# Kernel tuning notes

Measured on AMD Instinct MI355X. Metric: run time of the kernel, lower is better.

The kernel has to match this reference:

```python
import jax, jax.numpy as jnp
import numpy as np


def _parallel_scan_affine(log_a, b):
    """Hillis-Steele doubling scan for h_t = a_t*h_{t-1} + b_t (h_0 = 0).

    log_a, b: (B, T, d). Operator: (la2,b2) o (la1,b1) = (la1+la2, exp(la2)*b1 + b2).
    """
    T = log_a.shape[1]
    la, bv = log_a, b
    stride = 1
    while stride < T:  # static Python loop, log2(T) rounds
        la_prev = jnp.roll(la, stride, axis=1).at[:, :stride, :].set(0.0)
        bv_prev = jnp.roll(bv, stride, axis=1).at[:, :stride, :].set(0.0)
        bv = jnp.exp(la) * bv_prev + bv
        la = la + la_prev
        stride *= 2
    return bv


def setup_inputs() -> dict:
    key = jax.random.key(0)
    kx, kwz, kwh = jax.random.split(key, 3)
    B, T, D = 4, 4096, 1024
    x = jax.random.normal(kx, (B, T, D), dtype=jnp.float32)
    # nn.Linear(D, D) weights, stored as (out, in) like torch
    Wz = jax.random.normal(kwz, (D, D), dtype=jnp.float32) * 0.02
    bz = jnp.zeros((D,), dtype=jnp.float32)
    Wh = jax.random.normal(kwh, (D, D), dtype=jnp.float32) * 0.02
    bh = jnp.zeros((D,), dtype=jnp.float32)
    return {"x": x, "Wz": Wz, "bz": bz, "Wh": Wh, "bh": bh}


def reference(x, Wz, bz, Wh, bh):
    # forward_parallel: z = sigmoid(linear_z(x)); h_tilde = linear_h(x)
    z = jax.nn.sigmoid(jnp.einsum("btd,ed->bte", x, Wz) + bz)
    h_tilde = jnp.einsum("btd,ed->bte", x, Wh) + bh
    log_a = jnp.log(1.0 - z + 1e-08)
    b = z * h_tilde
    h_out = _parallel_scan_affine(log_a, b)
    return h_out  # out_proj is Identity since d_inner == d_model
```

## Files before the change

### kernel.cpp

```cpp
#include <hip/hip_runtime.h>
#include <hip/hip_bf16.h>


typedef __bf16 bf16x8 __attribute__((ext_vector_type(8)));
typedef __bf16 bf16x4 __attribute__((ext_vector_type(4)));
typedef float  f32x4  __attribute__((ext_vector_type(4)));

#define BSZ 4
#define TSZ 4096
#define DSZ 1024
#define MSZ (BSZ*TSZ)
#define CH  16
#define NC  (TSZ/CH)

__device__ __forceinline__ void gload_lds16(const __bf16* g, __bf16* l) {
  __builtin_amdgcn_global_load_lds(
      (const __attribute__((address_space(1))) void*)g,
      (__attribute__((address_space(3))) void*)l, 16, 0, 0);
}

__global__ void convert_tile_kernel(const float* __restrict__ X,
                                    const float* __restrict__ Wz,
                                    const float* __restrict__ Wh,
                                    __bf16* __restrict__ Xc,
                                    __bf16* __restrict__ Wzc,
                                    __bf16* __restrict__ Whc)
{
  const int bx = blockIdx.x;
  const float* src; __bf16* dst; int gid;
  if (bx < 8192)      { src = X;  dst = Xc;  gid =  bx        *256 + threadIdx.x; }
  else if (bx < 8704) { src = Wz; dst = Wzc; gid = (bx - 8192)*256 + threadIdx.x; }
  else                { src = Wh; dst = Whc; gid = (bx - 8704)*256 + threadIdx.x; }
  const int l    = gid & 63;
  const int i    = (gid >> 6) & 7;
  const int kblk = (gid >> 9) & 31;
  const int rblk = gid >> 14;
  const int row  = rblk*128 + i*16 + (l & 15);
  const int col  = kblk*32 + (l >> 4)*8;
  const float* g = src + (size_t)row*DSZ + col;
  float4 v0 = *(const float4*)g;
  float4 v1 = *(const float4*)(g + 4);
  bf16x8 p;
  p[0]=(__bf16)v0.x; p[1]=(__bf16)v0.y; p[2]=(__bf16)v0.z; p[3]=(__bf16)v0.w;
  p[4]=(__bf16)v1.x; p[5]=(__bf16)v1.y; p[6]=(__bf16)v1.z; p[7]=(__bf16)v1.w;
  *(bf16x8*)(dst + (size_t)gid*8) = p;
}

__global__ __launch_bounds__(256, 2) void gemm_gate_kernel(
    const __bf16* __restrict__ Xc,  const __bf16* __restrict__ Wzc,
    const __bf16* __restrict__ Whc,
    const float* __restrict__ bz, const float* __restrict__ bh,
    __bf16* __restrict__ a_ws, float* __restrict__ b_out,
    float* __restrict__ Aprod, float* __restrict__ Bcomp)
{
  __shared__ __align__(16) __bf16 As [8192];
  __shared__ __align__(16) __bf16 Bzs[8192];
  __shared__ __align__(16) __bf16 Bhs[8192];

  const int tid  = threadIdx.x;
  const int lane = tid & 63;
  const int wv   = tid >> 6;
  const int wM   = (wv >> 1) * 64;
  const int wN   = (wv & 1) * 64;
  const int wMg  = wM >> 4;
  const int wNg  = wN >> 4;
  const int lr   = lane & 15;
  const int q    = lane >> 4;
  const int wbase = wv * 64;

  const __bf16* Xb = Xc  + (size_t)blockIdx.x * 32 * 4096;
  const __bf16* Zb = Wzc + (size_t)blockIdx.y * 32 * 4096;
  const __bf16* Hb = Whc + (size_t)blockIdx.y * 32 * 4096;

  f32x4 accz[4][4] = {};
  f32x4 acch[4][4] = {};

  for (int kblk = 0; kblk < 16; ++kblk) {
    __syncthreads();
    const size_t tb = (size_t)kblk * 8192;
    #pragma unroll
    for (int c = 0; c < 4; ++c) {
      const int eo = (c*256 + wbase + lane) * 8;
      const int lo = (c*256 + wbase) * 8;
      gload_lds16(Xb + tb + eo, As  + lo);
      gload_lds16(Zb + tb + eo, Bzs + lo);
      gload_lds16(Hb + tb + eo, Bhs + lo);
    }
    __syncthreads();

    #pragma unroll
    for (int h = 0; h < 2; ++h) {
      const int ho = h * 4096;
      bf16x8 af[4];
      #pragma unroll
      for (int i = 0; i < 4; ++i)
        af[i] = *(const bf16x8*)(As + ho + (wMg + i)*512 + lane*8);
      #pragma unroll
      for (int j = 0; j < 4; ++j) {
        bf16x8 bz8 = *(const bf16x8*)(Bzs + ho + (wNg + j)*512 + lane*8);
        bf16x8 bh8 = *(const bf16x8*)(Bhs + ho + (wNg + j)*512 + lane*8);
        #pragma unroll
        for (int i = 0; i < 4; ++i) {
          accz[j][i] = __builtin_amdgcn_mfma_f32_16x16x32_bf16(af[i], bz8, accz[j][i], 0, 0, 0);
          acch[j][i] = __builtin_amdgcn_mfma_f32_16x16x32_bf16(af[i], bh8, acch[j][i], 0, 0, 0);
        }
      }
    }
  }

  const int M0 = blockIdx.x * 128;
  const int N0 = blockIdx.y * 128;
  #pragma unroll
  for (int j = 0; j < 4; ++j) {
    const int e = N0 + wN + j*16 + lr;
    const float bzv = bz[e];
    const float bhv = bh[e];
    float Aseg[4], Bseg[4];
    #pragma unroll
    for (int i = 0; i < 4; ++i) {
      const int mbase = M0 + wM + i*16 + q*4;
      float A = 1.0f, Bv = 0.0f;
      #pragma unroll
      for (int r = 0; r < 4; ++r) {
        const size_t idx = (size_t)(mbase + r)*DSZ + e;
        const float pz = accz[j][i][r] + bzv;
        const float ph = acch[j][i][r] + bhv;
        const float ex = __expf(-pz);
        const float z  = 1.0f / (1.0f + ex);
        const __bf16 abf = (__bf16)fmaf(ex, z, 1e-8f);
        const float  af  = (float)abf;
        const float  bf  = z * ph;
        a_ws[idx]  = abf;
        b_out[idx] = bf;
        Bv = fmaf(af, Bv, bf);
        A *= af;
      }
      Aseg[i] = A; Bseg[i] = Bv;
    }
    #pragma unroll
    for (int i = 0; i < 4; ++i) {
      #pragma unroll
      for (int s = 16; s < 64; s <<= 1) {
        const float Ap = __shfl_up(Aseg[i], s, 64);
        const float Bp = __shfl_up(Bseg[i], s, 64);
        if (lane >= s) { Bseg[i] = fmaf(Aseg[i], Bp, Bseg[i]); Aseg[i] *= Ap; }
      }
    }
    if (q == 3) {
      #pragma unroll
      for (int i = 0; i < 4; ++i) {
        const int bc = (M0 + wM + i*16) >> 4;
        Aprod[(size_t)bc*DSZ + e] = Aseg[i];
        Bcomp[(size_t)bc*DSZ + e] = Bseg[i];
      }
    }
  }
}

#define P2B 16
__global__ void scan_pass2_kernel(const float* Aprod,
                                  const float* __restrict__ Bcomp,
                                  float* Hstart)
{
  const int lane = threadIdx.x & 63;
  const int b    = blockIdx.x >> 4;
  const int d    = (blockIdx.x & 15) * 64 + lane;
  const size_t base = (size_t)b * NC * DSZ + d;
  float h = 0.0f;
  for (int c0 = 0; c0 < NC; c0 += P2B) {
    float Ar[P2B], Br[P2B];
    #pragma unroll
    for (int c = 0; c < P2B; ++c) {
      Ar[c] = Aprod[base + (size_t)(c0 + c)*DSZ];
      Br[c] = Bcomp[base + (size_t)(c0 + c)*DSZ];
    }
    #pragma unroll
    for (int c = 0; c < P2B; ++c) {
      Hstart[base + (size_t)(c0 + c)*DSZ] = h;
      h = fmaf(Ar[c], h, Br[c]);
    }
  }
}

__global__ void scan_pass3_kernel(const __bf16* __restrict__ a_ws,
                                  const float* __restrict__ Hstart,
                                  float* __restrict__ out)
{
  const int bc   = blockIdx.x;
  const int d0   = threadIdx.x * 4;
  const size_t base = (size_t)bc * CH * DSZ + d0;
  float4 hv = *(const float4*)(Hstart + (size_t)bc*DSZ + d0);
  float h[4] = {hv.x, hv.y, hv.z, hv.w};
  #pragma unroll
  for (int t = 0; t < CH; ++t) {
    bf16x4 a4 = *(const bf16x4*)(a_ws + base + (size_t)t*DSZ);
    float4 b4 = *(const float4*)(out + base + (size_t)t*DSZ);
    const float bb[4] = {b4.x, b4.y, b4.z, b4.w};
    #pragma unroll
    for (int c = 0; c < 4; ++c)
      h[c] = fmaf((float)a4[c], h[c], bb[c]);
    *(float4*)(out + base + (size_t)t*DSZ) = make_float4(h[0], h[1], h[2], h[3]);
  }
}

extern "C" void kernel_launch(void* const* d_in, const int* in_sizes, int n_in,
                              void* d_out, int out_size, void* d_ws, size_t ws_size,
                              hipStream_t stream)
{
  const float* x  = (const float*)d_in[0];
  const float* Wz = (const float*)d_in[1];
  const float* bz = (const float*)d_in[2];
  const float* Wh = (const float*)d_in[3];
  const float* bh = (const float*)d_in[4];
  float* out = (float*)d_out;

  __bf16* Xc   = (__bf16*)d_ws;
  __bf16* Wzc  = Xc  + (size_t)MSZ * DSZ;
  __bf16* Whc  = Wzc + (size_t)DSZ * DSZ;
  __bf16* a_ws = Whc + (size_t)DSZ * DSZ;
  float* Aprod  = (float*)(a_ws + (size_t)MSZ * DSZ);
  float* Bcomp  = Aprod + (size_t)BSZ*NC*DSZ;
  float* Hstart = Aprod;

  convert_tile_kernel<<<9216, 256, 0, stream>>>(x, Wz, Wh, Xc, Wzc, Whc);
  gemm_gate_kernel<<<dim3(MSZ/128, DSZ/128), 256, 0, stream>>>(
      Xc, Wzc, Whc, bz, bh, a_ws, out, Aprod, Bcomp);
  scan_pass2_kernel<<<64, 64, 0, stream>>>(Aprod, Bcomp, Hstart);
  scan_pass3_kernel<<<BSZ*NC, 256, 0, stream>>>(a_ws, Hstart, out);
}
```

Before: 241.3 us.

## Restructure gate GEMM into 256x256 double-buffered tiles with interleaved Wz/Wh

Wz and Wh are interleaved into one combined weight matrix in 16-row groups, so the GEMM treats the two projections as a single N=2048 product. The GEMM kernel moves to 512-thread blocks computing 256x256 tiles, with double-buffered LDS loads prefetched a step ahead and explicit vmcnt waits and barriers. It also raises MFMA priority with s_setprio and remaps block indices for L2 locality. This is meant to hide global-to-LDS latency and improve operand reuse, at the cost of more LDS (128KB per block), higher register pressure and hand-managed synchronisation that must be exactly right.

```diff
diff --git a/kernel.cpp b/kernel.cpp
--- a/kernel.cpp
+++ b/kernel.cpp
@@ -10,8 +10,12 @@
 #define TSZ 4096
 #define DSZ 1024
 #define MSZ (BSZ*TSZ)
+#define NSZ 2048
 #define CH  16
 #define NC  (TSZ/CH)
+
+#define BAR()  asm volatile("s_barrier" ::: "memory")
+#define VMW(n) asm volatile("s_waitcnt vmcnt(" #n ")" ::: "memory")
 
 __device__ __forceinline__ void gload_lds16(const __bf16* g, __bf16* l) {
   __builtin_amdgcn_global_load_lds(
@@ -23,19 +27,24 @@
                                     const float* __restrict__ Wz,
                                     const float* __restrict__ Wh,
                                     __bf16* __restrict__ Xc,
-                                    __bf16* __restrict__ Wzc,
-                                    __bf16* __restrict__ Whc)
+                                    __bf16* __restrict__ Wc)
 {
   const int bx = blockIdx.x;
-  const float* src; __bf16* dst; int gid;
-  if (bx < 8192)      { src = X;  dst = Xc;  gid =  bx        *256 + threadIdx.x; }
-  else if (bx < 8704) { src = Wz; dst = Wzc; gid = (bx - 8192)*256 + threadIdx.x; }
-  else                { src = Wh; dst = Whc; gid = (bx - 8704)*256 + threadIdx.x; }
+  const float* src; __bf16* dst; int gid; int row;
+  if (bx < 8192) {
+    gid = bx*256 + threadIdx.x;
+    const int l = gid & 63, i = (gid >> 6) & 7, rblk = gid >> 14;
+    row = rblk*128 + i*16 + (l & 15);
+    src = X; dst = Xc;
+  } else {
+    gid = (bx - 8192)*256 + threadIdx.x;
+    const int l = gid & 63, i = (gid >> 6) & 7, rblk = gid >> 14;
+    const int g = rblk*8 + i;
+    row = (g >> 1)*16 + (l & 15);
+    src = (g & 1) ? Wh : Wz; dst = Wc;
+  }
   const int l    = gid & 63;
-  const int i    = (gid >> 6) & 7;
   const int kblk = (gid >> 9) & 31;
-  const int rblk = gid >> 14;
-  const int row  = rblk*128 + i*16 + (l & 15);
   const int col  = kblk*32 + (l >> 4)*8;
   const float* g = src + (size_t)row*DSZ + col;
   float4 v0 = *(const float4*)g;
@@ -46,85 +55,147 @@
   *(bf16x8*)(dst + (size_t)gid*8) = p;
 }
 
-__global__ __launch_bounds__(256, 2) void gemm_gate_kernel(
-    const __bf16* __restrict__ Xc,  const __bf16* __restrict__ Wzc,
-    const __bf16* __restrict__ Whc,
+__global__ __launch_bounds__(512, 2) void gemm_gate_kernel(
+    const __bf16* __restrict__ Xc, const __bf16* __restrict__ Wc,
     const float* __restrict__ bz, const float* __restrict__ bh,
     __bf16* __restrict__ a_ws, float* __restrict__ b_out,
     float* __restrict__ Aprod, float* __restrict__ Bcomp)
 {
-  __shared__ __align__(16) __bf16 As [8192];
-  __shared__ __align__(16) __bf16 Bzs[8192];
-  __shared__ __align__(16) __bf16 Bhs[8192];
+  __shared__ __align__(16) __bf16 As[32768];
+  __shared__ __align__(16) __bf16 Bs[32768];
 
   const int tid  = threadIdx.x;
   const int lane = tid & 63;
-  const int wv   = tid >> 6;
-  const int wM   = (wv >> 1) * 64;
-  const int wN   = (wv & 1) * 64;
-  const int wMg  = wM >> 4;
-  const int wNg  = wN >> 4;
+  const int w    = tid >> 6;
+  const int wr   = w >> 2;
+  const int wc   = w & 3;
   const int lr   = lane & 15;
   const int q    = lane >> 4;
-  const int wbase = wv * 64;
-
-  const __bf16* Xb = Xc  + (size_t)blockIdx.x * 32 * 4096;
-  const __bf16* Zb = Wzc + (size_t)blockIdx.y * 32 * 4096;
-  const __bf16* Hb = Whc + (size_t)blockIdx.y * 32 * 4096;
-
-  f32x4 accz[4][4] = {};
-  f32x4 acch[4][4] = {};
-
-  for (int kblk = 0; kblk < 16; ++kblk) {
-    __syncthreads();
-    const size_t tb = (size_t)kblk * 8192;
-    #pragma unroll
-    for (int c = 0; c < 4; ++c) {
-      const int eo = (c*256 + wbase + lane) * 8;
-      const int lo = (c*256 + wbase) * 8;
-      gload_lds16(Xb + tb + eo, As  + lo);
-      gload_lds16(Zb + tb + eo, Bzs + lo);
-      gload_lds16(Hb + tb + eo, Bhs + lo);
-    }
-    __syncthreads();
-
-    #pragma unroll
-    for (int h = 0; h < 2; ++h) {
-      const int ho = h * 4096;
-      bf16x8 af[4];
-      #pragma unroll
-      for (int i = 0; i < 4; ++i)
-        af[i] = *(const bf16x8*)(As + ho + (wMg + i)*512 + lane*8);
-      #pragma unroll
-      for (int j = 0; j < 4; ++j) {
-        bf16x8 bz8 = *(const bf16x8*)(Bzs + ho + (wNg + j)*512 + lane*8);
-        bf16x8 bh8 = *(const bf16x8*)(Bhs + ho + (wNg + j)*512 + lane*8);
-        #pragma unroll
-        for (int i = 0; i < 4; ++i) {
-          accz[j][i] = __builtin_amdgcn_mfma_f32_16x16x32_bf16(af[i], bz8, accz[j][i], 0, 0, 0);
-          acch[j][i] = __builtin_amdgcn_mfma_f32_16x16x32_bf16(af[i], bh8, acch[j][i], 0, 0, 0);
-        }
-      }
-    }
-  }
-
-  const int M0 = blockIdx.x * 128;
-  const int N0 = blockIdx.y * 128;
-  #pragma unroll
-  for (int j = 0; j < 4; ++j) {
-    const int e = N0 + wN + j*16 + lr;
+
+  const int bid = blockIdx.x;
+  const int wg  = (bid & 7)*64 + (bid >> 3);
+  const int bx  = wg >> 3;
+  const int by  = wg & 7;
+
+  const int    lgo   = tid * 8;
+  const int    llo   = (tid >> 6) * 512;
+  const size_t xbase = (size_t)bx * 262144 + lgo;
+  const size_t wbase = (size_t)by * 262144 + lgo;
+  const int ard   = wr*4096 + lane*8;
+  const int bbase = (wc >> 1)*4096 + (wc & 1)*2048 + lane*8;
+
+  f32x4 acc[8][4] = {};
+  bf16x8 a4[4], b4[4];
+
+  #pragma unroll
+  for (int h = 0; h < 2; ++h) gload_lds16(Xc + xbase + h*131072 + 0*4096, As + 0*8192 + h*4096 + llo);
+  #pragma unroll
+  for (int h = 0; h < 2; ++h) gload_lds16(Wc + wbase + h*131072 + 0*4096, Bs + 0*8192 + h*4096 + llo);
+  #pragma unroll
+  for (int h = 0; h < 2; ++h) gload_lds16(Xc + xbase + h*131072 + 1*4096, As + 1*8192 + h*4096 + llo);
+  #pragma unroll
+  for (int h = 0; h < 2; ++h) gload_lds16(Wc + wbase + h*131072 + 1*4096, Bs + 1*8192 + h*4096 + llo);
+  VMW(4);
+  BAR();
+
+  for (int t = 0; t < 16; ++t) {
+    const int cur = t & 1, nxt = cur ^ 1;
+    const int cb0 = (cur*2 + 0)*8192;
+    const int cb1 = (cur*2 + 1)*8192;
+    const int nb0 = (nxt*2 + 0)*8192;
+    const int nb1 = (nxt*2 + 1)*8192;
+    const size_t g0 = (size_t)(2*t + 2) * 4096;
+    const size_t g1 = (size_t)(2*t + 3) * 4096;
+
+    #pragma unroll
+    for (int m = 0; m < 4; ++m) a4[m] = *(const bf16x8*)(As + cb0 + ard + m*512);
+    #pragma unroll
+    for (int j = 0; j < 4; ++j) b4[j] = *(const bf16x8*)(Bs + cb0 + bbase + j*512);
+    if (t < 15) {
+      #pragma unroll
+      for (int h = 0; h < 2; ++h) gload_lds16(Xc + xbase + h*131072 + g0, As + nb0 + h*4096 + llo);
+    }
+    BAR();
+    __builtin_amdgcn_s_setprio(1);
+    #pragma unroll
+    for (int j = 0; j < 4; ++j)
+      #pragma unroll
+      for (int m = 0; m < 4; ++m)
+        acc[m][j] = __builtin_amdgcn_mfma_f32_16x16x32_bf16(a4[m], b4[j], acc[m][j], 0, 0, 0);
+    __builtin_amdgcn_s_setprio(0);
+    BAR();
+
+    #pragma unroll
+    for (int m = 0; m < 4; ++m) a4[m] = *(const bf16x8*)(As + cb0 + ard + (4+m)*512);
+    if (t < 15) {
+      #pragma unroll
+      for (int h = 0; h < 2; ++h) gload_lds16(Wc + wbase + h*131072 + g0, Bs + nb0 + h*4096 + llo);
+      VMW(4);
+    } else {
+      VMW(0);
+    }
+    BAR();
+    __builtin_amdgcn_s_setprio(1);
+    #pragma unroll
+    for (int j = 0; j < 4; ++j)
+      #pragma unroll
+      for (int m = 0; m < 4; ++m)
+        acc[4+m][j] = __builtin_amdgcn_mfma_f32_16x16x32_bf16(a4[m], b4[j], acc[4+m][j], 0, 0, 0);
+    __builtin_amdgcn_s_setprio(0);
+    BAR();
+
+    #pragma unroll
+    for (int m = 0; m < 4; ++m) a4[m] = *(const bf16x8*)(As + cb1 + ard + m*512);
+    #pragma unroll
+    for (int j = 0; j < 4; ++j) b4[j] = *(const bf16x8*)(Bs + cb1 + bbase + j*512);
+    if (t < 15) {
+      #pragma unroll
+      for (int h = 0; h < 2; ++h) gload_lds16(Xc + xbase + h*131072 + g1, As + nb1 + h*4096 + llo);
+    }
+    BAR();
+    __builtin_amdgcn_s_setprio(1);
+    #pragma unroll
+    for (int j = 0; j < 4; ++j)
+      #pragma unroll
+      for (int m = 0; m < 4; ++m)
+        acc[m][j] = __builtin_amdgcn_mfma_f32_16x16x32_bf16(a4[m], b4[j], acc[m][j], 0, 0, 0);
+    __builtin_amdgcn_s_setprio(0);
+    BAR();
+
+    #pragma unroll
+    for (int m = 0; m < 4; ++m) a4[m] = *(const bf16x8*)(As + cb1 + ard + (4+m)*512);
+    if (t < 15) {
+      #pragma unroll
+      for (int h = 0; h < 2; ++h) gload_lds16(Wc + wbase + h*131072 + g1, Bs + nb1 + h*4096 + llo);
+      VMW(4);
+    }
+    BAR();
+    __builtin_amdgcn_s_setprio(1);
+    #pragma unroll
+    for (int j = 0; j < 4; ++j)
+      #pragma unroll
+      for (int m = 0; m < 4; ++m)
+        acc[4+m][j] = __builtin_amdgcn_mfma_f32_16x16x32_bf16(a4[m], b4[j], acc[4+m][j], 0, 0, 0);
+    __builtin_amdgcn_s_setprio(0);
+    BAR();
+  }
+
+  const int rowb = bx*256 + wr*128;
+  #pragma unroll
+  for (int u = 0; u < 2; ++u) {
+    const int e = (by*8 + wc*2 + u)*16 + lr;
     const float bzv = bz[e];
     const float bhv = bh[e];
-    float Aseg[4], Bseg[4];
-    #pragma unroll
-    for (int i = 0; i < 4; ++i) {
-      const int mbase = M0 + wM + i*16 + q*4;
+    float Aseg[8], Bseg[8];
+    #pragma unroll
+    for (int m = 0; m < 8; ++m) {
+      const int mbase = rowb + m*16 + q*4;
       float A = 1.0f, Bv = 0.0f;
       #pragma unroll
       for (int r = 0; r < 4; ++r) {
         const size_t idx = (size_t)(mbase + r)*DSZ + e;
-        const float pz = accz[j][i][r] + bzv;
-        const float ph = acch[j][i][r] + bhv;
+        const float pz = acc[m][2*u][r]   + bzv;
+        const float ph = acc[m][2*u+1][r] + bhv;
         const float ex = __expf(-pz);
         const float z  = 1.0f / (1.0f + ex);
         const __bf16 abf = (__bf16)fmaf(ex, z, 1e-8f);
@@ -135,23 +206,23 @@
         Bv = fmaf(af, Bv, bf);
         A *= af;
       }
-      Aseg[i] = A; Bseg[i] = Bv;
-    }
-    #pragma unroll
-    for (int i = 0; i < 4; ++i) {
+      Aseg[m] = A; Bseg[m] = Bv;
+    }
+    #pragma unroll
+    for (int m = 0; m < 8; ++m) {
       #pragma unroll
       for (int s = 16; s < 64; s <<= 1) {
-        const float Ap = __shfl_up(Aseg[i], s, 64);
-        const float Bp = __shfl_up(Bseg[i], s, 64);
-        if (lane >= s) { Bseg[i] = fmaf(Aseg[i], Bp, Bseg[i]); Aseg[i] *= Ap; }
+        const float Ap = __shfl_up(Aseg[m], s, 64);
+        const float Bp = __shfl_up(Bseg[m], s, 64);
+        if (lane >= s) { Bseg[m] = fmaf(Aseg[m], Bp, Bseg[m]); Aseg[m] *= Ap; }
       }
     }
     if (q == 3) {
       #pragma unroll
-      for (int i = 0; i < 4; ++i) {
-        const int bc = (M0 + wM + i*16) >> 4;
-        Aprod[(size_t)bc*DSZ + e] = Aseg[i];
-        Bcomp[(size_t)bc*DSZ + e] = Bseg[i];
+      for (int m = 0; m < 8; ++m) {
+        const int bc = (rowb + m*16) >> 4;
+        Aprod[(size_t)bc*DSZ + e] = Aseg[m];
+        Bcomp[(size_t)bc*DSZ + e] = Bseg[m];
       }
     }
   }
@@ -215,16 +286,14 @@
   float* out = (float*)d_out;
 
   __bf16* Xc   = (__bf16*)d_ws;
-  __bf16* Wzc  = Xc  + (size_t)MSZ * DSZ;
-  __bf16* Whc  = Wzc + (size_t)DSZ * DSZ;
-  __bf16* a_ws = Whc + (size_t)DSZ * DSZ;
+  __bf16* Wc   = Xc + (size_t)MSZ * DSZ;
+  __bf16* a_ws = Wc + (size_t)NSZ * DSZ;
   float* Aprod  = (float*)(a_ws + (size_t)MSZ * DSZ);
   float* Bcomp  = Aprod + (size_t)BSZ*NC*DSZ;
   float* Hstart = Aprod;
 
-  convert_tile_kernel<<<9216, 256, 0, stream>>>(x, Wz, Wh, Xc, Wzc, Whc);
-  gemm_gate_kernel<<<dim3(MSZ/128, DSZ/128), 256, 0, stream>>>(
-      Xc, Wzc, Whc, bz, bh, a_ws, out, Aprod, Bcomp);
+  convert_tile_kernel<<<9216, 256, 0, stream>>>(x, Wz, Wh, Xc, Wc);
+  gemm_gate_kernel<<<512, 512, 0, stream>>>(Xc, Wc, bz, bh, a_ws, out, Aprod, Bcomp);
   scan_pass2_kernel<<<64, 64, 0, stream>>>(Aprod, Bcomp, Hstart);
   scan_pass3_kernel<<<BSZ*NC, 256, 0, stream>>>(a_ws, Hstart, out);
 }
```

Result: no change. 243.6 us (+0.9%).
